# Performance work log

Measured on AMD Instinct MI355X. Metric: run time of the kernel, lower is better.

Reference implementation:

```python
import jax, jax.numpy as jnp
import numpy as np

# Block sizes (dst node counts per layer, dst nodes are prefix of src nodes)
NUM_DST = (61952, 5632, 512)


def _sage_layer(h, esrc, edst, num_dst, W_self, W_neigh, b):
    # DGL SAGEConv with 'mean' aggregator (eval mode, no dropout):
    # out = h_dst @ W_self + mean_{neighbors}(h_src) @ W_neigh + b
    h_dst = h[:num_dst]
    msg = h[esrc]                                              # [E, d] gather
    agg = jax.ops.segment_sum(msg, edst, num_segments=num_dst)  # [num_dst, d]
    deg = jax.ops.segment_sum(jnp.ones((esrc.shape[0],), h.dtype), edst,
                              num_segments=num_dst)
    mean = agg / jnp.maximum(deg, 1.0)[:, None]
    return h_dst @ W_self + mean @ W_neigh + b


def setup_inputs() -> dict:
    key = jax.random.key(0)
    ks = jax.random.split(key, 16)
    N_SRC = (681472, 61952, 5632)
    E = (619520, 56320, 5120)
    IN, HID, NC = 256, 256, 19
    inp = {}
    inp['x'] = jax.random.normal(ks[0], (N_SRC[0], IN), dtype=jnp.float32)
    for i in range(3):
        inp[f'esrc{i}'] = jax.random.randint(ks[1 + 2 * i], (E[i],), 0, N_SRC[i])
        inp[f'edst{i}'] = jax.random.randint(ks[2 + 2 * i], (E[i],), 0, NUM_DST[i])
    dims = [(IN, HID), (HID, HID), (HID, NC)]
    for i, (di, do) in enumerate(dims):
        s = 1.0 / np.sqrt(di)
        inp[f'W_self{i}'] = jax.random.normal(ks[7 + 3 * i], (di, do), dtype=jnp.float32) * s
        inp[f'W_neigh{i}'] = jax.random.normal(ks[8 + 3 * i], (di, do), dtype=jnp.float32) * s
        inp[f'b{i}'] = jnp.zeros((do,), dtype=jnp.float32)
    return inp


def reference(x, esrc0, edst0, esrc1, edst1, esrc2, edst2,
              W_self0, W_neigh0, b0, W_self1, W_neigh1, b1,
              W_self2, W_neigh2, b2) -> jnp.ndarray:
    h = _sage_layer(x, esrc0, edst0, NUM_DST[0], W_self0, W_neigh0, b0)
    h = jax.nn.relu(h)  # dropout is identity in eval
    h = _sage_layer(h, esrc1, edst1, NUM_DST[1], W_self1, W_neigh1, b1)
    h = jax.nn.relu(h)
    h = _sage_layer(h, esrc2, edst2, NUM_DST[2], W_self2, W_neigh2, b2)
    return h
```

## Files before the change

### kernel.cpp

```cpp
#include <hip/hip_runtime.h>
#include <hip/hip_bf16.h>

#define HID 256
#define NC  19


__global__ void hist_kernel(const int* __restrict__ edst, int E, int* __restrict__ deg) {
    int i = blockIdx.x * blockDim.x + threadIdx.x;
    if (i < E) atomicAdd(&deg[edst[i]], 1);
}

__global__ void scanA_kernel(const int* __restrict__ deg, int* __restrict__ offs,
                             int* __restrict__ bsums, int n) {
    __shared__ int s[256];
    int i = blockIdx.x * 256 + threadIdx.x;
    int v = (i < n) ? deg[i] : 0;
    s[threadIdx.x] = v;
    __syncthreads();
    for (int d = 1; d < 256; d <<= 1) {
        int t = (threadIdx.x >= d) ? s[threadIdx.x - d] : 0;
        __syncthreads();
        s[threadIdx.x] += t;
        __syncthreads();
    }
    if (i < n) offs[i] = s[threadIdx.x] - v;
    if (threadIdx.x == 255) bsums[blockIdx.x] = s[255];
}

__global__ void scanB_kernel(int* __restrict__ bsums, int nb) {
    __shared__ int s[256];
    int v = (threadIdx.x < nb) ? bsums[threadIdx.x] : 0;
    s[threadIdx.x] = v;
    __syncthreads();
    for (int d = 1; d < 256; d <<= 1) {
        int t = (threadIdx.x >= d) ? s[threadIdx.x - d] : 0;
        __syncthreads();
        s[threadIdx.x] += t;
        __syncthreads();
    }
    if (threadIdx.x < nb) bsums[threadIdx.x] = s[threadIdx.x] - v;
}

__global__ void scanC_kernel(int* __restrict__ offs, const int* __restrict__ bsums,
                             int* __restrict__ cursor, int n) {
    int i = blockIdx.x * 256 + threadIdx.x;
    if (i < n) {
        int o = offs[i] + bsums[blockIdx.x];
        offs[i] = o;
        cursor[i] = o;
    }
}

__global__ void scatter_kernel(const int* __restrict__ esrc, const int* __restrict__ edst,
                               int E, int* __restrict__ cursor, int* __restrict__ eidx) {
    int i = blockIdx.x * blockDim.x + threadIdx.x;
    if (i < E) {
        int d = edst[i];
        int pos = atomicAdd(&cursor[d], 1);
        eidx[pos] = esrc[i];
    }
}

__global__ void aggregate_kernel(const int* __restrict__ eidx, const int* __restrict__ offs,
                                 const int* __restrict__ deg, const float* __restrict__ hsrc,
                                 float* __restrict__ mean, int ndst) {
    int d = blockIdx.x * 4 + (threadIdx.x >> 6);
    int lane = threadIdx.x & 63;
    if (d >= ndst) return;
    int start = offs[d];
    int cnt = deg[d];
    float4 acc = make_float4(0.f, 0.f, 0.f, 0.f);
    for (int e = 0; e < cnt; ++e) {
        int s = eidx[start + e];
        float4 v = *reinterpret_cast<const float4*>(hsrc + (size_t)s * HID + lane * 4);
        acc.x += v.x; acc.y += v.y; acc.z += v.z; acc.w += v.w;
    }
    float inv = 1.0f / (float)(cnt > 1 ? cnt : 1);
    acc.x *= inv; acc.y *= inv; acc.z *= inv; acc.w *= inv;
    *reinterpret_cast<float4*>(mean + (size_t)d * HID + lane * 4) = acc;
}

template <bool RELU>
__global__ __launch_bounds__(256) void sage_gemm(
    const float* __restrict__ hdst, const float* __restrict__ mean,
    const float* __restrict__ Wself, const float* __restrict__ Wneigh,
    const float* __restrict__ bias, float* __restrict__ out, int M) {
    __shared__ float As[16][128];
    __shared__ float Bs[16][64];
    const int tid = threadIdx.x;
    const int m0 = blockIdx.x * 128;
    const int c0 = blockIdx.y * 64;

    const int aRow = tid >> 1;
    const int aK   = (tid & 1) * 8;
    const int bK   = tid >> 4;
    const int bN   = (tid & 15) * 4;
    const int tx   = tid & 15;
    const int ty   = tid >> 4;

    const float4* As4 = reinterpret_cast<const float4*>(&As[0][0]);
    const float4* Bs4 = reinterpret_cast<const float4*>(&Bs[0][0]);

    float acc[8][4];
#pragma unroll
    for (int i = 0; i < 8; ++i)
#pragma unroll
        for (int j = 0; j < 4; ++j) acc[i][j] = 0.f;

    for (int kt = 0; kt < 32; ++kt) {
        const int k = kt * 16;
        const float* Abase = (k < 256)
            ? hdst + (size_t)(m0 + aRow) * HID + (k + aK)
            : mean + (size_t)(m0 + aRow) * HID + (k - 256 + aK);
        float4 av0 = *reinterpret_cast<const float4*>(Abase);
        float4 av1 = *reinterpret_cast<const float4*>(Abase + 4);
        const float* Bbase = (k < 256)
            ? Wself  + (size_t)(k + bK) * HID + (c0 + bN)
            : Wneigh + (size_t)(k - 256 + bK) * HID + (c0 + bN);
        float4 bv = *reinterpret_cast<const float4*>(Bbase);

        __syncthreads();
        As[aK + 0][aRow] = av0.x; As[aK + 1][aRow] = av0.y;
        As[aK + 2][aRow] = av0.z; As[aK + 3][aRow] = av0.w;
        As[aK + 4][aRow] = av1.x; As[aK + 5][aRow] = av1.y;
        As[aK + 6][aRow] = av1.z; As[aK + 7][aRow] = av1.w;
        *reinterpret_cast<float4*>(&Bs[bK][bN]) = bv;
        __syncthreads();

#pragma unroll
        for (int kk = 0; kk < 16; ++kk) {
            float4 a0 = As4[kk * 32 + ty * 2];
            float4 a1 = As4[kk * 32 + ty * 2 + 1];
            float4 b  = Bs4[kk * 16 + tx];
            float ar[8] = {a0.x, a0.y, a0.z, a0.w, a1.x, a1.y, a1.z, a1.w};
            float br[4] = {b.x, b.y, b.z, b.w};
#pragma unroll
            for (int i = 0; i < 8; ++i)
#pragma unroll
                for (int j = 0; j < 4; ++j) acc[i][j] += ar[i] * br[j];
        }
    }

    float4 b4 = *reinterpret_cast<const float4*>(bias + c0 + tx * 4);
    float bb[4] = {b4.x, b4.y, b4.z, b4.w};
#pragma unroll
    for (int i = 0; i < 8; ++i) {
        float4 o;
        float* op = &o.x;
#pragma unroll
        for (int j = 0; j < 4; ++j) {
            float v = acc[i][j] + bb[j];
            if (RELU) v = fmaxf(v, 0.f);
            op[j] = v;
        }
        *reinterpret_cast<float4*>(out + (size_t)(m0 + ty * 8 + i) * HID + c0 + tx * 4) = o;
    }
}

__global__ void out_gemm(const float* __restrict__ hdst, const float* __restrict__ mean,
                         const float* __restrict__ Wself, const float* __restrict__ Wneigh,
                         const float* __restrict__ bias, float* __restrict__ out) {
    int r = blockIdx.x;
    int lane = threadIdx.x;
    if (lane >= NC) return;
    const float* hr = hdst + (size_t)r * HID;
    const float* mr = mean + (size_t)r * HID;
    float s0 = 0.f, s1 = 0.f, s2 = 0.f, s3 = 0.f;
    for (int k = 0; k < HID; k += 4) {
        s0 = fmaf(hr[k],     Wself[(k)     * NC + lane], s0);
        s1 = fmaf(hr[k + 1], Wself[(k + 1) * NC + lane], s1);
        s2 = fmaf(hr[k + 2], Wself[(k + 2) * NC + lane], s2);
        s3 = fmaf(hr[k + 3], Wself[(k + 3) * NC + lane], s3);
    }
    for (int k = 0; k < HID; k += 4) {
        s0 = fmaf(mr[k],     Wneigh[(k)     * NC + lane], s0);
        s1 = fmaf(mr[k + 1], Wneigh[(k + 1) * NC + lane], s1);
        s2 = fmaf(mr[k + 2], Wneigh[(k + 2) * NC + lane], s2);
        s3 = fmaf(mr[k + 3], Wneigh[(k + 3) * NC + lane], s3);
    }
    out[r * NC + lane] = s0 + s1 + s2 + s3 + bias[lane];
}


extern "C" void kernel_launch(void* const* d_in, const int* in_sizes, int n_in,
                              void* d_out, int out_size, void* d_ws, size_t ws_size,
                              hipStream_t stream) {
    const float* x     = (const float*)d_in[0];
    const int* esrc0   = (const int*)d_in[1];
    const int* edst0   = (const int*)d_in[2];
    const int* esrc1   = (const int*)d_in[3];
    const int* edst1   = (const int*)d_in[4];
    const int* esrc2   = (const int*)d_in[5];
    const int* edst2   = (const int*)d_in[6];
    const float* Ws0   = (const float*)d_in[7];
    const float* Wn0   = (const float*)d_in[8];
    const float* b0    = (const float*)d_in[9];
    const float* Ws1   = (const float*)d_in[10];
    const float* Wn1   = (const float*)d_in[11];
    const float* b1    = (const float*)d_in[12];
    const float* Ws2   = (const float*)d_in[13];
    const float* Wn2   = (const float*)d_in[14];
    const float* b2    = (const float*)d_in[15];

    const int NDST0 = 61952, NDST1 = 5632, NDST2 = 512;
    const int E0 = in_sizes[1], E1 = in_sizes[3], E2 = in_sizes[5];

    char* ws = (char*)d_ws;
    size_t off = 0;
    auto alloc = [&](size_t bytes) -> void* {
        void* p = ws + off;
        off += (bytes + 255) & ~(size_t)255;
        return p;
    };
    float* mean0 = (float*)alloc((size_t)NDST0 * HID * 4);
    float* h1    = (float*)alloc((size_t)NDST0 * HID * 4);
    float* mean1 = (float*)alloc((size_t)NDST1 * HID * 4);
    float* h2    = (float*)alloc((size_t)NDST1 * HID * 4);
    float* mean2 = (float*)alloc((size_t)NDST2 * HID * 4);
    int* eidx    = (int*)alloc((size_t)E0 * 4);
    int* deg     = (int*)alloc((size_t)NDST0 * 4);
    int* offs    = (int*)alloc((size_t)NDST0 * 4);
    int* cursor  = (int*)alloc((size_t)NDST0 * 4);
    int* bsums   = (int*)alloc(1024);

    auto run_csr_mean = [&](const float* hsrc, const int* esrc, const int* edst,
                            int E, int ndst, float* mean) {
        hipMemsetAsync(deg, 0, (size_t)ndst * 4, stream);
        hist_kernel<<<dim3((E + 255) / 256), dim3(256), 0, stream>>>(edst, E, deg);
        int nb = (ndst + 255) / 256;
        scanA_kernel<<<dim3(nb), dim3(256), 0, stream>>>(deg, offs, bsums, ndst);
        scanB_kernel<<<dim3(1), dim3(256), 0, stream>>>(bsums, nb);
        scanC_kernel<<<dim3(nb), dim3(256), 0, stream>>>(offs, bsums, cursor, ndst);
        scatter_kernel<<<dim3((E + 255) / 256), dim3(256), 0, stream>>>(esrc, edst, E, cursor, eidx);
        aggregate_kernel<<<dim3((ndst + 3) / 4), dim3(256), 0, stream>>>(eidx, offs, deg, hsrc, mean, ndst);
    };

    run_csr_mean(x, esrc0, edst0, E0, NDST0, mean0);
    sage_gemm<true><<<dim3(NDST0 / 128, 4), dim3(256), 0, stream>>>(x, mean0, Ws0, Wn0, b0, h1, NDST0);

    run_csr_mean(h1, esrc1, edst1, E1, NDST1, mean1);
    sage_gemm<true><<<dim3(NDST1 / 128, 4), dim3(256), 0, stream>>>(h1, mean1, Ws1, Wn1, b1, h2, NDST1);

    run_csr_mean(h2, esrc2, edst2, E2, NDST2, mean2);
    out_gemm<<<dim3(512), dim3(64), 0, stream>>>(h2, mean2, Ws2, Wn2, b2, (float*)d_out);
}
```

Before: 1.322 ms.

## Replace FP32 SIMT GEMM with split-bf16 MFMA GEMM for hidden layers

```diff
diff --git a/kernel.cpp b/kernel.cpp
--- a/kernel.cpp
+++ b/kernel.cpp
@@ -3,6 +3,18 @@
 
 #define HID 256
 #define NC  19
+
+typedef short short8 __attribute__((ext_vector_type(8)));
+typedef float f32x4 __attribute__((ext_vector_type(4)));
+
+__device__ __forceinline__ unsigned short f2bf(float f) {
+    unsigned int u = __float_as_uint(f);
+    u = (u + 0x7fffu + ((u >> 16) & 1u)) >> 16;
+    return (unsigned short)u;
+}
+__device__ __forceinline__ float bf2f(unsigned short h) {
+    return __uint_as_float(((unsigned int)h) << 16);
+}
 
 
 __global__ void hist_kernel(const int* __restrict__ edst, int E, int* __restrict__ deg) {
@@ -61,99 +73,149 @@
     }
 }
 
+template <bool BF16OUT>
 __global__ void aggregate_kernel(const int* __restrict__ eidx, const int* __restrict__ offs,
                                  const int* __restrict__ deg, const float* __restrict__ hsrc,
-                                 float* __restrict__ mean, int ndst) {
+                                 float* __restrict__ meanf, unsigned short* __restrict__ mh,
+                                 unsigned short* __restrict__ ml, int ndst) {
     int d = blockIdx.x * 4 + (threadIdx.x >> 6);
     int lane = threadIdx.x & 63;
     if (d >= ndst) return;
     int start = offs[d];
     int cnt = deg[d];
-    float4 acc = make_float4(0.f, 0.f, 0.f, 0.f);
-    for (int e = 0; e < cnt; ++e) {
-        int s = eidx[start + e];
-        float4 v = *reinterpret_cast<const float4*>(hsrc + (size_t)s * HID + lane * 4);
-        acc.x += v.x; acc.y += v.y; acc.z += v.z; acc.w += v.w;
+    float ax = 0.f, ay = 0.f, az = 0.f, aw = 0.f;
+    int e = 0;
+    for (; e + 2 <= cnt; e += 2) {
+        int s0 = eidx[start + e];
+        int s1 = eidx[start + e + 1];
+        float4 v0 = *reinterpret_cast<const float4*>(hsrc + (size_t)s0 * HID + lane * 4);
+        float4 v1 = *reinterpret_cast<const float4*>(hsrc + (size_t)s1 * HID + lane * 4);
+        ax += v0.x + v1.x; ay += v0.y + v1.y; az += v0.z + v1.z; aw += v0.w + v1.w;
+    }
+    if (e < cnt) {
+        int s0 = eidx[start + e];
+        float4 v0 = *reinterpret_cast<const float4*>(hsrc + (size_t)s0 * HID + lane * 4);
+        ax += v0.x; ay += v0.y; az += v0.z; aw += v0.w;
     }
     float inv = 1.0f / (float)(cnt > 1 ? cnt : 1);
-    acc.x *= inv; acc.y *= inv; acc.z *= inv; acc.w *= inv;
-    *reinterpret_cast<float4*>(mean + (size_t)d * HID + lane * 4) = acc;
-}
+    ax *= inv; ay *= inv; az *= inv; aw *= inv;
+    if (BF16OUT) {
+        ushort4 h, l;
+        h.x = f2bf(ax); l.x = f2bf(ax - bf2f(h.x));
+        h.y = f2bf(ay); l.y = f2bf(ay - bf2f(h.y));
+        h.z = f2bf(az); l.z = f2bf(az - bf2f(h.z));
+        h.w = f2bf(aw); l.w = f2bf(aw - bf2f(h.w));
+        *reinterpret_cast<ushort4*>(mh + (size_t)d * HID + lane * 4) = h;
+        *reinterpret_cast<ushort4*>(ml + (size_t)d * HID + lane * 4) = l;
+    } else {
+        float4 o = make_float4(ax, ay, az, aw);
+        *reinterpret_cast<float4*>(meanf + (size_t)d * HID + lane * 4) = o;
+    }
+}
+
+__global__ void conv_rows(const float* __restrict__ src, unsigned short* __restrict__ hi,
+                          unsigned short* __restrict__ lo, int n4) {
+    int i = blockIdx.x * 256 + threadIdx.x;
+    if (i >= n4) return;
+    float4 v = reinterpret_cast<const float4*>(src)[i];
+    ushort4 h, l;
+    h.x = f2bf(v.x); l.x = f2bf(v.x - bf2f(h.x));
+    h.y = f2bf(v.y); l.y = f2bf(v.y - bf2f(h.y));
+    h.z = f2bf(v.z); l.z = f2bf(v.z - bf2f(h.z));
+    h.w = f2bf(v.w); l.w = f2bf(v.w - bf2f(h.w));
+    reinterpret_cast<ushort4*>(hi)[i] = h;
+    reinterpret_cast<ushort4*>(lo)[i] = l;
+}
+
+__global__ void prep_w(const float* __restrict__ Ws0, const float* __restrict__ Wn0,
+                       const float* __restrict__ Ws1, const float* __restrict__ Wn1,
+                       unsigned short* __restrict__ wth, unsigned short* __restrict__ wtl) {
+    int idx = blockIdx.x * 256 + threadIdx.x;
+    int layer = idx >> 17;
+    int t = idx & 131071;
+    int n = t >> 9;
+    int k = t & 511;
+    const float* Ws = layer ? Ws1 : Ws0;
+    const float* Wn = layer ? Wn1 : Wn0;
+    float v = (k < 256) ? Ws[k * 256 + n] : Wn[(k - 256) * 256 + n];
+    unsigned short h = f2bf(v);
+    unsigned short l = f2bf(v - bf2f(h));
+    wth[idx] = h;
+    wtl[idx] = l;
+}
+
+#define MFMA16(A, B)                                                                   \
+    _Pragma("unroll") for (int mi = 0; mi < 4; ++mi)                                   \
+        _Pragma("unroll") for (int ni = 0; ni < 4; ++ni)                               \
+            acc[mi][ni] = __builtin_amdgcn_mfma_f32_16x16x32_bf16(A[mi], B[ni],        \
+                                                                  acc[mi][ni], 0, 0, 0);
 
 template <bool RELU>
-__global__ __launch_bounds__(256) void sage_gemm(
-    const float* __restrict__ hdst, const float* __restrict__ mean,
-    const float* __restrict__ Wself, const float* __restrict__ Wneigh,
+__global__ __launch_bounds__(256, 2) void mfma_gemm(
+    const unsigned short* __restrict__ Ahd, const unsigned short* __restrict__ Ald,
+    const unsigned short* __restrict__ Ahm, const unsigned short* __restrict__ Alm,
+    const unsigned short* __restrict__ Wh, const unsigned short* __restrict__ Wl,
     const float* __restrict__ bias, float* __restrict__ out, int M) {
-    __shared__ float As[16][128];
-    __shared__ float Bs[16][64];
-    const int tid = threadIdx.x;
-    const int m0 = blockIdx.x * 128;
-    const int c0 = blockIdx.y * 64;
-
-    const int aRow = tid >> 1;
-    const int aK   = (tid & 1) * 8;
-    const int bK   = tid >> 4;
-    const int bN   = (tid & 15) * 4;
-    const int tx   = tid & 15;
-    const int ty   = tid >> 4;
-
-    const float4* As4 = reinterpret_cast<const float4*>(&As[0][0]);
-    const float4* Bs4 = reinterpret_cast<const float4*>(&Bs[0][0]);
-
-    float acc[8][4];
-#pragma unroll
-    for (int i = 0; i < 8; ++i)
-#pragma unroll
-        for (int j = 0; j < 4; ++j) acc[i][j] = 0.f;
-
-    for (int kt = 0; kt < 32; ++kt) {
-        const int k = kt * 16;
-        const float* Abase = (k < 256)
-            ? hdst + (size_t)(m0 + aRow) * HID + (k + aK)
-            : mean + (size_t)(m0 + aRow) * HID + (k - 256 + aK);
-        float4 av0 = *reinterpret_cast<const float4*>(Abase);
-        float4 av1 = *reinterpret_cast<const float4*>(Abase + 4);
-        const float* Bbase = (k < 256)
-            ? Wself  + (size_t)(k + bK) * HID + (c0 + bN)
-            : Wneigh + (size_t)(k - 256 + bK) * HID + (c0 + bN);
-        float4 bv = *reinterpret_cast<const float4*>(Bbase);
-
-        __syncthreads();
-        As[aK + 0][aRow] = av0.x; As[aK + 1][aRow] = av0.y;
-        As[aK + 2][aRow] = av0.z; As[aK + 3][aRow] = av0.w;
-        As[aK + 4][aRow] = av1.x; As[aK + 5][aRow] = av1.y;
-        As[aK + 6][aRow] = av1.z; As[aK + 7][aRow] = av1.w;
-        *reinterpret_cast<float4*>(&Bs[bK][bN]) = bv;
-        __syncthreads();
-
-#pragma unroll
-        for (int kk = 0; kk < 16; ++kk) {
-            float4 a0 = As4[kk * 32 + ty * 2];
-            float4 a1 = As4[kk * 32 + ty * 2 + 1];
-            float4 b  = Bs4[kk * 16 + tx];
-            float ar[8] = {a0.x, a0.y, a0.z, a0.w, a1.x, a1.y, a1.z, a1.w};
-            float br[4] = {b.x, b.y, b.z, b.w};
-#pragma unroll
-            for (int i = 0; i < 8; ++i)
-#pragma unroll
-                for (int j = 0; j < 4; ++j) acc[i][j] += ar[i] * br[j];
+    const int lane = threadIdx.x & 63;
+    const int w = threadIdx.x >> 6;
+    const int wr = w >> 1, wc = w & 1;
+    const int r0 = blockIdx.x * 128 + wr * 64;
+    const int c0 = blockIdx.y * 128 + wc * 64;
+    const int lrow = lane & 15;
+    const int lkg8 = (lane >> 4) * 8;
+
+    size_t aoff[4], boff[4];
+#pragma unroll
+    for (int mi = 0; mi < 4; ++mi) aoff[mi] = (size_t)(r0 + mi * 16 + lrow) * HID + lkg8;
+#pragma unroll
+    for (int ni = 0; ni < 4; ++ni) boff[ni] = (size_t)(c0 + ni * 16 + lrow) * 512 + lkg8;
+
+    f32x4 acc[4][4];
+#pragma unroll
+    for (int mi = 0; mi < 4; ++mi)
+#pragma unroll
+        for (int ni = 0; ni < 4; ++ni) acc[mi][ni] = (f32x4)(0.f);
+
+    auto getA = [&](int s, int mi) -> short8 {
+        int k512 = (s & 15) * 32;
+        const unsigned short* plane =
+            (s < 32) ? (k512 < 256 ? Ahd : Ahm) : (k512 < 256 ? Ald : Alm);
+        return *reinterpret_cast<const short8*>(plane + aoff[mi] + (k512 & 255));
+    };
+    auto getB = [&](int s, int ni) -> short8 {
+        const unsigned short* plane = (s & 16) ? Wl : Wh;
+        return *reinterpret_cast<const short8*>(plane + boff[ni] + (s & 15) * 32);
+    };
+
+    short8 a0[4], b0[4], a1[4], b1[4];
+#pragma unroll
+    for (int i = 0; i < 4; ++i) { a0[i] = getA(0, i); b0[i] = getB(0, i); }
+
+    for (int s = 0; s < 64; s += 2) {
+#pragma unroll
+        for (int i = 0; i < 4; ++i) { a1[i] = getA(s + 1, i); b1[i] = getB(s + 1, i); }
+        MFMA16(a0, b0);
+        if (s + 2 < 64) {
+#pragma unroll
+            for (int i = 0; i < 4; ++i) { a0[i] = getA(s + 2, i); b0[i] = getB(s + 2, i); }
         }
-    }
-
-    float4 b4 = *reinterpret_cast<const float4*>(bias + c0 + tx * 4);
-    float bb[4] = {b4.x, b4.y, b4.z, b4.w};
-#pragma unroll
-    for (int i = 0; i < 8; ++i) {
-        float4 o;
-        float* op = &o.x;
-#pragma unroll
-        for (int j = 0; j < 4; ++j) {
-            float v = acc[i][j] + bb[j];
-            if (RELU) v = fmaxf(v, 0.f);
-            op[j] = v;
+        MFMA16(a1, b1);
+    }
+
+#pragma unroll
+    for (int ni = 0; ni < 4; ++ni) {
+        int col = c0 + ni * 16 + lrow;
+        float bv = bias[col];
+#pragma unroll
+        for (int mi = 0; mi < 4; ++mi) {
+            int row0 = r0 + mi * 16 + (lane >> 4) * 4;
+#pragma unroll
+            for (int j = 0; j < 4; ++j) {
+                float v = acc[mi][ni][j] + bv;
+                if (RELU) v = fmaxf(v, 0.f);
+                out[(size_t)(row0 + j) * HID + col] = v;
+            }
         }
-        *reinterpret_cast<float4*>(out + (size_t)(m0 + ty * 8 + i) * HID + c0 + tx * 4) = o;
     }
 }
 
@@ -185,22 +247,22 @@
 extern "C" void kernel_launch(void* const* d_in, const int* in_sizes, int n_in,
                               void* d_out, int out_size, void* d_ws, size_t ws_size,
                               hipStream_t stream) {
-    const float* x     = (const float*)d_in[0];
-    const int* esrc0   = (const int*)d_in[1];
-    const int* edst0   = (const int*)d_in[2];
-    const int* esrc1   = (const int*)d_in[3];
-    const int* edst1   = (const int*)d_in[4];
-    const int* esrc2   = (const int*)d_in[5];
-    const int* edst2   = (const int*)d_in[6];
-    const float* Ws0   = (const float*)d_in[7];
-    const float* Wn0   = (const float*)d_in[8];
-    const float* b0    = (const float*)d_in[9];
-    const float* Ws1   = (const float*)d_in[10];
-    const float* Wn1   = (const float*)d_in[11];
-    const float* b1    = (const float*)d_in[12];
-    const float* Ws2   = (const float*)d_in[13];
-    const float* Wn2   = (const float*)d_in[14];
-    const float* b2    = (const float*)d_in[15];
+    const float* x   = (const float*)d_in[0];
+    const int* esrc0 = (const int*)d_in[1];
+    const int* edst0 = (const int*)d_in[2];
+    const int* esrc1 = (const int*)d_in[3];
+    const int* edst1 = (const int*)d_in[4];
+    const int* esrc2 = (const int*)d_in[5];
+    const int* edst2 = (const int*)d_in[6];
+    const float* Ws0 = (const float*)d_in[7];
+    const float* Wn0 = (const float*)d_in[8];
+    const float* b0  = (const float*)d_in[9];
+    const float* Ws1 = (const float*)d_in[10];
+    const float* Wn1 = (const float*)d_in[11];
+    const float* b1  = (const float*)d_in[12];
+    const float* Ws2 = (const float*)d_in[13];
+    const float* Wn2 = (const float*)d_in[14];
+    const float* b2  = (const float*)d_in[15];
 
     const int NDST0 = 61952, NDST1 = 5632, NDST2 = 512;
     const int E0 = in_sizes[1], E1 = in_sizes[3], E2 = in_sizes[5];
@@ -212,19 +274,26 @@
         off += (bytes + 255) & ~(size_t)255;
         return p;
     };
-    float* mean0 = (float*)alloc((size_t)NDST0 * HID * 4);
+    unsigned short* xh  = (unsigned short*)alloc((size_t)NDST0 * HID * 2);
+    unsigned short* xl  = (unsigned short*)alloc((size_t)NDST0 * HID * 2);
+    unsigned short* mh0 = (unsigned short*)alloc((size_t)NDST0 * HID * 2);
+    unsigned short* ml0 = (unsigned short*)alloc((size_t)NDST0 * HID * 2);
+    unsigned short* h1h = (unsigned short*)alloc((size_t)NDST1 * HID * 2);
+    unsigned short* h1l = (unsigned short*)alloc((size_t)NDST1 * HID * 2);
+    unsigned short* mh1 = (unsigned short*)alloc((size_t)NDST1 * HID * 2);
+    unsigned short* ml1 = (unsigned short*)alloc((size_t)NDST1 * HID * 2);
+    unsigned short* wth = (unsigned short*)alloc((size_t)2 * 256 * 512 * 2);
+    unsigned short* wtl = (unsigned short*)alloc((size_t)2 * 256 * 512 * 2);
     float* h1    = (float*)alloc((size_t)NDST0 * HID * 4);
-    float* mean1 = (float*)alloc((size_t)NDST1 * HID * 4);
     float* h2    = (float*)alloc((size_t)NDST1 * HID * 4);
     float* mean2 = (float*)alloc((size_t)NDST2 * HID * 4);
-    int* eidx    = (int*)alloc((size_t)E0 * 4);
-    int* deg     = (int*)alloc((size_t)NDST0 * 4);
-    int* offs    = (int*)alloc((size_t)NDST0 * 4);
-    int* cursor  = (int*)alloc((size_t)NDST0 * 4);
-    int* bsums   = (int*)alloc(1024);
-
-    auto run_csr_mean = [&](const float* hsrc, const int* esrc, const int* edst,
-                            int E, int ndst, float* mean) {
+    int* eidx   = (int*)alloc((size_t)E0 * 4);
+    int* deg    = (int*)alloc((size_t)NDST0 * 4);
+    int* offs   = (int*)alloc((size_t)NDST0 * 4);
+    int* cursor = (int*)alloc((size_t)NDST0 * 4);
+    int* bsums  = (int*)alloc(1024);
+
+    auto run_csr = [&](const int* esrc, const int* edst, int E, int ndst) {
         hipMemsetAsync(deg, 0, (size_t)ndst * 4, stream);
         hist_kernel<<<dim3((E + 255) / 256), dim3(256), 0, stream>>>(edst, E, deg);
         int nb = (ndst + 255) / 256;
@@ -232,15 +301,26 @@
         scanB_kernel<<<dim3(1), dim3(256), 0, stream>>>(bsums, nb);
         scanC_kernel<<<dim3(nb), dim3(256), 0, stream>>>(offs, bsums, cursor, ndst);
         scatter_kernel<<<dim3((E + 255) / 256), dim3(256), 0, stream>>>(esrc, edst, E, cursor, eidx);
-        aggregate_kernel<<<dim3((ndst + 3) / 4), dim3(256), 0, stream>>>(eidx, offs, deg, hsrc, mean, ndst);
     };
 
-    run_csr_mean(x, esrc0, edst0, E0, NDST0, mean0);
-    sage_gemm<true><<<dim3(NDST0 / 128, 4), dim3(256), 0, stream>>>(x, mean0, Ws0, Wn0, b0, h1, NDST0);
-
-    run_csr_mean(h1, esrc1, edst1, E1, NDST1, mean1);
-    sage_gemm<true><<<dim3(NDST1 / 128, 4), dim3(256), 0, stream>>>(h1, mean1, Ws1, Wn1, b1, h2, NDST1);
-
-    run_csr_mean(h2, esrc2, edst2, E2, NDST2, mean2);
+    prep_w<<<dim3(1024), dim3(256), 0, stream>>>(Ws0, Wn0, Ws1, Wn1, wth, wtl);
+    conv_rows<<<dim3(NDST0 * HID / 4 / 256), dim3(256), 0, stream>>>(x, xh, xl, NDST0 * HID / 4);
+
+    run_csr(esrc0, edst0, E0, NDST0);
+    aggregate_kernel<true><<<dim3((NDST0 + 3) / 4), dim3(256), 0, stream>>>(
+        eidx, offs, deg, x, nullptr, mh0, ml0, NDST0);
+    mfma_gemm<true><<<dim3(NDST0 / 128, 2), dim3(256), 0, stream>>>(
+        xh, xl, mh0, ml0, wth, wtl, b0, h1, NDST0);
+
+    conv_rows<<<dim3(NDST1 * HID / 4 / 256), dim3(256), 0, stream>>>(h1, h1h, h1l, NDST1 * HID / 4);
+    run_csr(esrc1, edst1, E1, NDST1);
+    aggregate_kernel<true><<<dim3((NDST1 + 3) / 4), dim3(256), 0, stream>>>(
+        eidx, offs, deg, h1, nullptr, mh1, ml1, NDST1);
+    mfma_gemm<true><<<dim3(NDST1 / 128, 2), dim3(256), 0, stream>>>(
+        h1h, h1l, mh1, ml1, wth + 131072, wtl + 131072, b1, h2, NDST1);
+
+    run_csr(esrc2, edst2, E2, NDST2);
+    aggregate_kernel<false><<<dim3((NDST2 + 3) / 4), dim3(256), 0, stream>>>(
+        eidx, offs, deg, h2, mean2, nullptr, nullptr, NDST2);
     out_gemm<<<dim3(512), dim3(64), 0, stream>>>(h2, mean2, Ws2, Wn2, b2, (float*)d_out);
 }
```

Result: slower. 1.444 ms (+9.2%).
